# Kernel optimization log

Measured on AMD Instinct MI355X. Metric: run time of the kernel, lower is better.

The kernel has to match this reference:

```python
import jax, jax.numpy as jnp
import numpy as np

MATRIX_DIM = 128
FEAT = MATRIX_DIM * (MATRIX_DIM + 1) // 2  # 8256, triu incl. diagonal
HID = FEAT // 5                            # 1651
BATCH = 4096


def setup_inputs() -> dict:
    key = jax.random.key(0)
    k0, k1, k2, k3, k4 = jax.random.split(key, 5)
    stdv1 = 1.0 / FEAT / 2.0
    stdv2 = 1.0 / HID / 2.0
    return {
        "sim_matrices": jax.random.normal(k0, (BATCH, MATRIX_DIM, MATRIX_DIM), dtype=jnp.float32),
        "W1": jax.random.uniform(k1, (HID, FEAT), minval=-stdv1, maxval=stdv1, dtype=jnp.float32),
        "b1": jax.random.uniform(k2, (HID,), minval=-stdv1, maxval=stdv1, dtype=jnp.float32),
        "W2": jax.random.uniform(k3, (1, HID), minval=-stdv2, maxval=stdv2, dtype=jnp.float32),
        "b2": jax.random.uniform(k4, (1,), minval=-stdv2, maxval=stdv2, dtype=jnp.float32),
    }


def reference(sim_matrices, W1, b1, W2, b2):
    # flatten: take upper-triangular (incl. diag) entries -> [B, FEAT]
    iu0, iu1 = np.triu_indices(sim_matrices.shape[1])
    x = sim_matrices[:, iu0, iu1]
    # Linear_block 1 (ideal crossbar VMM = W x + b) + ReLU
    h = jax.nn.relu(jnp.einsum("bf,hf->bh", x, W1) + b1)
    # Linear_block 2 + Sigmoid -> [B, 1]
    return jax.nn.sigmoid(jnp.einsum("bh,oh->bo", h, W2) + b2)
```

## Files before the change

### kernel.cpp

```cpp
#include <hip/hip_runtime.h>
#include <hip/hip_bf16.h>
#include <math.h>

#define MDIM  128
#define FEAT  8256
#define HID   1651
#define HIDP  1664
#define BATCH 4096
#define BK    64
#define KT_TOTAL 129
#define NCHUNK 516
#define W1SCALE 8192.0f
#define W1INV   (1.0f / 8192.0f)
#define DEPTH 3

#define XT_CSTRIDE  ((i64)BATCH * 16)
#define W1T_CSTRIDE ((i64)HIDP * 16)

using f32x4  = __attribute__((ext_vector_type(4))) float;
using f32x16 = __attribute__((ext_vector_type(16))) float;
using i32x4  = __attribute__((ext_vector_type(4))) int;
using i32x8  = __attribute__((ext_vector_type(8))) int;
typedef long long i64;

__device__ __forceinline__ void gload_lds16(const void* g, void* l) {
    __builtin_amdgcn_global_load_lds(
        (const __attribute__((address_space(1))) void*)g,
        (__attribute__((address_space(3))) void*)l,
        16, 0, 0);
}

__device__ __forceinline__ int row_off(int i) { return (i * (257 - i)) >> 1; }

__device__ __forceinline__ void pack8_fp8(const float* f, int* o) {
    int lo = __builtin_amdgcn_cvt_pk_fp8_f32(f[0], f[1], 0, false);
    lo     = __builtin_amdgcn_cvt_pk_fp8_f32(f[2], f[3], lo, true);
    int hi = __builtin_amdgcn_cvt_pk_fp8_f32(f[4], f[5], 0, false);
    hi     = __builtin_amdgcn_cvt_pk_fp8_f32(f[6], f[7], hi, true);
    o[0] = lo; o[1] = hi;
}

__global__ void __launch_bounds__(256)
prep_kernel(const float* __restrict__ sim, const float* __restrict__ W1,
            char* __restrict__ Xt, char* __restrict__ W1t,
            float* __restrict__ out_pre) {
    const int t = threadIdx.x;
    if (blockIdx.x < BATCH) {
        const int b = blockIdx.x;
        const float* srow = sim + ((i64)b << 14);
#pragma unroll
        for (int it = 0; it < 5; ++it) {
            const int g = it * 256 + t;
            if (g < FEAT / 8) {
                const int f0 = g * 8;
                int i = (int)((257.0f - sqrtf(66049.0f - 8.0f * (float)f0)) * 0.5f);
                i = i < 0 ? 0 : (i > 127 ? 127 : i);
                while (i < 127 && row_off(i + 1) <= f0) ++i;
                while (i > 0 && row_off(i) > f0) --i;
                int j = i + (f0 - row_off(i));
                float v[8];
#pragma unroll
                for (int e = 0; e < 8; ++e) {
                    if (j > 127) { ++i; j = i; }
                    v[e] = srow[i * MDIM + j];
                    ++j;
                }
                int o[2];
                pack8_fp8(v, o);
                *(int2*)(Xt + (i64)(g >> 1) * XT_CSTRIDE + (i64)b * 16
                            + (g & 1) * 8) = make_int2(o[0], o[1]);
            }
        }
    } else if (blockIdx.x < BATCH + 5 * HIDP) {
        const int c  = blockIdx.x - BATCH;
        const int wb = c % 5;
        const int n  = c / 5;
        const int g  = wb * 256 + t;
        if (g >= FEAT / 8) return;
        const int f0 = g * 8;
        int o[2];
        if (n < HID) {
            const float* src = W1 + (i64)n * FEAT + f0;
            const f32x4 a = *(const f32x4*)src;
            const f32x4 d = *(const f32x4*)(src + 4);
            float v[8];
#pragma unroll
            for (int e = 0; e < 4; ++e) {
                v[e]     = a[e] * W1SCALE;
                v[e + 4] = d[e] * W1SCALE;
            }
            pack8_fp8(v, o);
        } else {
            o[0] = 0; o[1] = 0;
        }
        *(int2*)(W1t + (i64)(g >> 1) * W1T_CSTRIDE + (i64)n * 16
                    + (g & 1) * 8) = make_int2(o[0], o[1]);
    } else {
        const f32x4 zz = {0.f, 0.f, 0.f, 0.f};
        f32x4* p = (f32x4*)out_pre + t * 4;
        p[0] = zz; p[1] = zz; p[2] = zz; p[3] = zz;
    }
}

__global__ void __launch_bounds__(256, 3)
gemm_fused_kernel(const char* __restrict__ Xt,
                  const char* __restrict__ W1t,
                  const float* __restrict__ b1,
                  const float* __restrict__ W2,
                  float* __restrict__ out_pre) {
    __shared__ __align__(16) char lds_a[DEPTH * 8192];
    __shared__ __align__(16) char lds_b[DEPTH * 8192];

    const int t    = threadIdx.x;
    const int w    = t >> 6;
    const int l    = t & 63;
    const int bm   = blockIdx.x;
    const int bn   = blockIdx.y;
    const int wm   = w >> 1;
    const int wn   = w & 1;
    const int lm   = l & 31;
    const int c0   = (l >> 5) << 1;

    f32x16 acc[2][2];
#pragma unroll
    for (int r = 0; r < 16; ++r) {
        acc[0][0][r] = 0.f; acc[0][1][r] = 0.f;
        acc[1][0][r] = 0.f; acc[1][1][r] = 0.f;
    }

    const int nkt = KT_TOTAL;

    const char* gA0 = Xt + (i64)(w >> 1) * XT_CSTRIDE
                         + ((i64)bm * 128 + (w & 1) * 64 + l) * 16;
    const char* gB0 = W1t + (i64)(w >> 1) * W1T_CSTRIDE
                          + ((i64)bn * 128 + (w & 1) * 64 + l) * 16;
    char* lA = lds_a + w * 1024;
    char* lB = lds_b + w * 1024;

#define STAGE(buf, kidx) do {                                             \
        const char* _ga = gA0 + (i64)(kidx) * (4 * XT_CSTRIDE);           \
        const char* _gb = gB0 + (i64)(kidx) * (4 * W1T_CSTRIDE);          \
        char* _la = lA + (buf) * 8192;                                    \
        char* _lb = lB + (buf) * 8192;                                    \
        gload_lds16(_ga,                    _la);                         \
        gload_lds16(_ga + 2 * XT_CSTRIDE,   _la + 4096);                  \
        gload_lds16(_gb,                    _lb);                         \
        gload_lds16(_gb + 2 * W1T_CSTRIDE,  _lb + 4096);                  \
    } while (0)

    STAGE(0, 0);
    STAGE(1, 1);
    STAGE(2, 2);

    int cur = 0;
    for (int kt = 0; kt < nkt; ++kt) {
        if (kt + 3 <= nkt)      asm volatile("s_waitcnt vmcnt(8)" ::: "memory");
        else if (kt + 2 == nkt) asm volatile("s_waitcnt vmcnt(4)" ::: "memory");
        else                    asm volatile("s_waitcnt vmcnt(0)" ::: "memory");
        __builtin_amdgcn_s_barrier();
        __builtin_amdgcn_sched_barrier(0);

        const char* pa = lds_a + cur * 8192 + c0 * 2048 + (wm * 64 + lm) * 16;
        const char* pb = lds_b + cur * 8192 + c0 * 2048 + (wn * 64 + lm) * 16;
        i32x8 A0, A1, B0, B1;
        *((i32x4*)&A0)     = *(const i32x4*)(pa);
        *((i32x4*)&A0 + 1) = *(const i32x4*)(pa + 2048);
        *((i32x4*)&A1)     = *(const i32x4*)(pa + 512);
        *((i32x4*)&A1 + 1) = *(const i32x4*)(pa + 512 + 2048);
        *((i32x4*)&B0)     = *(const i32x4*)(pb);
        *((i32x4*)&B0 + 1) = *(const i32x4*)(pb + 2048);
        *((i32x4*)&B1)     = *(const i32x4*)(pb + 512);
        *((i32x4*)&B1 + 1) = *(const i32x4*)(pb + 512 + 2048);

        __builtin_amdgcn_s_setprio(1);
        acc[0][0] = __builtin_amdgcn_mfma_scale_f32_32x32x64_f8f6f4(
            A0, B0, acc[0][0], 0, 0, 0, 0x7F7F7F7F, 0, 0x7F7F7F7F);
        acc[0][1] = __builtin_amdgcn_mfma_scale_f32_32x32x64_f8f6f4(
            A0, B1, acc[0][1], 0, 0, 0, 0x7F7F7F7F, 0, 0x7F7F7F7F);
        acc[1][0] = __builtin_amdgcn_mfma_scale_f32_32x32x64_f8f6f4(
            A1, B0, acc[1][0], 0, 0, 0, 0x7F7F7F7F, 0, 0x7F7F7F7F);
        acc[1][1] = __builtin_amdgcn_mfma_scale_f32_32x32x64_f8f6f4(
            A1, B1, acc[1][1], 0, 0, 0, 0x7F7F7F7F, 0, 0x7F7F7F7F);
        __builtin_amdgcn_s_setprio(0);

        asm volatile("s_waitcnt lgkmcnt(0)" ::: "memory");
        __builtin_amdgcn_sched_barrier(0);
        __builtin_amdgcn_s_barrier();
        __builtin_amdgcn_sched_barrier(0);

        if (kt + 3 < nkt) STAGE(cur, kt + 3);
        cur = (cur == DEPTH - 1) ? 0 : cur + 1;
    }
#undef STAGE

    const int colbase = bn * 128 + wn * 64 + lm;
    float b1v[2], w2v[2];
#pragma unroll
    for (int cb = 0; cb < 2; ++cb) {
        const int col = colbase + cb * 32;
        const bool ok = col < HID;
        b1v[cb] = ok ? b1[col] : 0.f;
        w2v[cb] = ok ? W2[col] : 0.f;
    }
    const int rbase = bm * 128 + wm * 64 + ((l >> 5) << 2);
#pragma unroll
    for (int rb = 0; rb < 2; ++rb)
#pragma unroll
        for (int reg = 0; reg < 16; ++reg) {
            float v = 0.f;
#pragma unroll
            for (int cb = 0; cb < 2; ++cb) {
                const float pre = acc[rb][cb][reg] * W1INV + b1v[cb];
                v += fmaxf(pre, 0.f) * w2v[cb];
            }
            v += __shfl_xor(v, 1);
            v += __shfl_xor(v, 2);
            v += __shfl_xor(v, 4);
            v += __shfl_xor(v, 8);
            v += __shfl_xor(v, 16);
            if (lm == 0) {
                const int row = rbase + rb * 32 + (reg & 3) + ((reg >> 2) << 3);
                atomicAdd(out_pre + row, v);
            }
        }
}

__global__ void __launch_bounds__(256)
sigmoid_kernel(const float* __restrict__ pre,
               const float* __restrict__ b2,
               float* __restrict__ out) {
    const int i = blockIdx.x * 256 + threadIdx.x;
    out[i] = 1.0f / (1.0f + expf(-(pre[i] + b2[0])));
}

extern "C" void kernel_launch(void* const* d_in, const int* in_sizes, int n_in,
                              void* d_out, int out_size, void* d_ws, size_t ws_size,
                              hipStream_t stream) {
    const float* sim = (const float*)d_in[0];
    const float* W1  = (const float*)d_in[1];
    const float* b1  = (const float*)d_in[2];
    const float* W2  = (const float*)d_in[3];
    const float* b2  = (const float*)d_in[4];
    float* out = (float*)d_out;

    char* ws = (char*)d_ws;
    const i64 X_OFF   = 0;
    const i64 W1P_OFF = (i64)BATCH * FEAT;
    const i64 PRE_OFF = W1P_OFF + (i64)HIDP * FEAT;
    char*  Xt   = ws + X_OFF;
    char*  W1t  = ws + W1P_OFF;
    float* pre  = (float*)(ws + PRE_OFF);

    prep_kernel<<<BATCH + 5 * HIDP + 1, 256, 0, stream>>>(sim, W1, Xt, W1t, pre);
    {
        dim3 grid(BATCH / 128, HIDP / 128);
        gemm_fused_kernel<<<grid, 256, 0, stream>>>(Xt, W1t, b1, W2, pre);
    }
    sigmoid_kernel<<<BATCH / 256, 256, 0, stream>>>(pre, b2, out);
}
```

Before: 482.8 us.

## Load A operand directly to registers in MFMA-fragment layout, bypassing LDS

The prep kernel now writes the fp8 activation matrix in a layout where each wave's MFMA A fragment is contiguous per k-step. The GEMM kernel loads A straight from global memory into registers, triple-buffered two k-steps ahead, while only B still goes through LDS. This halves LDS traffic and footprint and drops the A LDS round trip. In exchange it depends on global load latency being hidden by register prefetch, and it adds VGPR pressure from six extra 8-wide register buffers.

```diff
diff --git a/kernel.cpp b/kernel.cpp
--- a/kernel.cpp
+++ b/kernel.cpp
@@ -9,13 +9,11 @@
 #define BATCH 4096
 #define BK    64
 #define KT_TOTAL 129
-#define NCHUNK 516
 #define W1SCALE 8192.0f
 #define W1INV   (1.0f / 8192.0f)
-#define DEPTH 3
-
-#define XT_CSTRIDE  ((i64)BATCH * 16)
+
 #define W1T_CSTRIDE ((i64)HIDP * 16)
+#define XA_KSTEP ((i64)128 * 2048)
 
 using f32x4  = __attribute__((ext_vector_type(4))) float;
 using f32x16 = __attribute__((ext_vector_type(16))) float;
@@ -42,12 +40,14 @@
 
 __global__ void __launch_bounds__(256)
 prep_kernel(const float* __restrict__ sim, const float* __restrict__ W1,
-            char* __restrict__ Xt, char* __restrict__ W1t,
+            char* __restrict__ XA, char* __restrict__ W1t,
             float* __restrict__ out_pre) {
     const int t = threadIdx.x;
     if (blockIdx.x < BATCH) {
         const int b = blockIdx.x;
         const float* srow = sim + ((i64)b << 14);
+        const int mg   = b >> 5;
+        const int brow = b & 31;
 #pragma unroll
         for (int it = 0; it < 5; ++it) {
             const int g = it * 256 + t;
@@ -67,8 +67,13 @@
                 }
                 int o[2];
                 pack8_fp8(v, o);
-                *(int2*)(Xt + (i64)(g >> 1) * XT_CSTRIDE + (i64)b * 16
-                            + (g & 1) * 8) = make_int2(o[0], o[1]);
+                const int kt   = f0 >> 6;
+                const int k64  = f0 & 63;
+                const int lane = brow | ((k64 >> 5) << 5);
+                const int h    = (k64 >> 4) & 1;
+                const i64 off  = ((i64)(kt * 128 + mg) * 2 + h) * 1024
+                               + lane * 16 + (k64 & 15);
+                *(int2*)(XA + off) = make_int2(o[0], o[1]);
             }
         }
     } else if (blockIdx.x < BATCH + 5 * HIDP) {
@@ -103,13 +108,12 @@
 }
 
 __global__ void __launch_bounds__(256, 3)
-gemm_fused_kernel(const char* __restrict__ Xt,
+gemm_fused_kernel(const char* __restrict__ XA,
                   const char* __restrict__ W1t,
                   const float* __restrict__ b1,
                   const float* __restrict__ W2,
                   float* __restrict__ out_pre) {
-    __shared__ __align__(16) char lds_a[DEPTH * 8192];
-    __shared__ __align__(16) char lds_b[DEPTH * 8192];
+    __shared__ __align__(16) char lds_b[3 * 8192];
 
     const int t    = threadIdx.x;
     const int w    = t >> 6;
@@ -128,70 +132,81 @@
         acc[1][0][r] = 0.f; acc[1][1][r] = 0.f;
     }
 
-    const int nkt = KT_TOTAL;
-
-    const char* gA0 = Xt + (i64)(w >> 1) * XT_CSTRIDE
-                         + ((i64)bm * 128 + (w & 1) * 64 + l) * 16;
+    const char* pA0 = XA + (i64)(bm * 4 + wm * 2) * 2048 + l * 16;
+
     const char* gB0 = W1t + (i64)(w >> 1) * W1T_CSTRIDE
                           + ((i64)bn * 128 + (w & 1) * 64 + l) * 16;
-    char* lA = lds_a + w * 1024;
     char* lB = lds_b + w * 1024;
 
-#define STAGE(buf, kidx) do {                                             \
-        const char* _ga = gA0 + (i64)(kidx) * (4 * XT_CSTRIDE);           \
+#define STAGE_B(slot, kidx) do {                                          \
         const char* _gb = gB0 + (i64)(kidx) * (4 * W1T_CSTRIDE);          \
-        char* _la = lA + (buf) * 8192;                                    \
-        char* _lb = lB + (buf) * 8192;                                    \
-        gload_lds16(_ga,                    _la);                         \
-        gload_lds16(_ga + 2 * XT_CSTRIDE,   _la + 4096);                  \
-        gload_lds16(_gb,                    _lb);                         \
-        gload_lds16(_gb + 2 * W1T_CSTRIDE,  _lb + 4096);                  \
-    } while (0)
-
-    STAGE(0, 0);
-    STAGE(1, 1);
-    STAGE(2, 2);
-
-    int cur = 0;
-    for (int kt = 0; kt < nkt; ++kt) {
-        if (kt + 3 <= nkt)      asm volatile("s_waitcnt vmcnt(8)" ::: "memory");
-        else if (kt + 2 == nkt) asm volatile("s_waitcnt vmcnt(4)" ::: "memory");
-        else                    asm volatile("s_waitcnt vmcnt(0)" ::: "memory");
-        __builtin_amdgcn_s_barrier();
-        __builtin_amdgcn_sched_barrier(0);
-
-        const char* pa = lds_a + cur * 8192 + c0 * 2048 + (wm * 64 + lm) * 16;
-        const char* pb = lds_b + cur * 8192 + c0 * 2048 + (wn * 64 + lm) * 16;
-        i32x8 A0, A1, B0, B1;
-        *((i32x4*)&A0)     = *(const i32x4*)(pa);
-        *((i32x4*)&A0 + 1) = *(const i32x4*)(pa + 2048);
-        *((i32x4*)&A1)     = *(const i32x4*)(pa + 512);
-        *((i32x4*)&A1 + 1) = *(const i32x4*)(pa + 512 + 2048);
-        *((i32x4*)&B0)     = *(const i32x4*)(pb);
-        *((i32x4*)&B0 + 1) = *(const i32x4*)(pb + 2048);
-        *((i32x4*)&B1)     = *(const i32x4*)(pb + 512);
-        *((i32x4*)&B1 + 1) = *(const i32x4*)(pb + 512 + 2048);
-
-        __builtin_amdgcn_s_setprio(1);
-        acc[0][0] = __builtin_amdgcn_mfma_scale_f32_32x32x64_f8f6f4(
-            A0, B0, acc[0][0], 0, 0, 0, 0x7F7F7F7F, 0, 0x7F7F7F7F);
-        acc[0][1] = __builtin_amdgcn_mfma_scale_f32_32x32x64_f8f6f4(
-            A0, B1, acc[0][1], 0, 0, 0, 0x7F7F7F7F, 0, 0x7F7F7F7F);
-        acc[1][0] = __builtin_amdgcn_mfma_scale_f32_32x32x64_f8f6f4(
-            A1, B0, acc[1][0], 0, 0, 0, 0x7F7F7F7F, 0, 0x7F7F7F7F);
-        acc[1][1] = __builtin_amdgcn_mfma_scale_f32_32x32x64_f8f6f4(
-            A1, B1, acc[1][1], 0, 0, 0, 0x7F7F7F7F, 0, 0x7F7F7F7F);
-        __builtin_amdgcn_s_setprio(0);
-
-        asm volatile("s_waitcnt lgkmcnt(0)" ::: "memory");
-        __builtin_amdgcn_sched_barrier(0);
-        __builtin_amdgcn_s_barrier();
-        __builtin_amdgcn_sched_barrier(0);
-
-        if (kt + 3 < nkt) STAGE(cur, kt + 3);
-        cur = (cur == DEPTH - 1) ? 0 : cur + 1;
-    }
-#undef STAGE
+        char* _lb = lB + (slot) * 8192;                                   \
+        gload_lds16(_gb,                   _lb);                          \
+        gload_lds16(_gb + 2 * W1T_CSTRIDE, _lb + 4096);                   \
+    } while (0)
+
+#define LOAD_A(kt, an0, an1) do {                                         \
+        const char* _pa = pA0 + (i64)(kt) * XA_KSTEP;                     \
+        *((i32x4*)&(an0))     = *(const i32x4*)(_pa);                     \
+        *((i32x4*)&(an0) + 1) = *(const i32x4*)(_pa + 1024);              \
+        *((i32x4*)&(an1))     = *(const i32x4*)(_pa + 2048);              \
+        *((i32x4*)&(an1) + 1) = *(const i32x4*)(_pa + 3072);              \
+    } while (0)
+
+#define MFMA4(a0, a1, B0, B1) do {                                        \
+        __builtin_amdgcn_s_setprio(1);                                    \
+        acc[0][0] = __builtin_amdgcn_mfma_scale_f32_32x32x64_f8f6f4(      \
+            (a0), (B0), acc[0][0], 0, 0, 0, 0x7F7F7F7F, 0, 0x7F7F7F7F);   \
+        acc[0][1] = __builtin_amdgcn_mfma_scale_f32_32x32x64_f8f6f4(      \
+            (a0), (B1), acc[0][1], 0, 0, 0, 0x7F7F7F7F, 0, 0x7F7F7F7F);   \
+        acc[1][0] = __builtin_amdgcn_mfma_scale_f32_32x32x64_f8f6f4(      \
+            (a1), (B0), acc[1][0], 0, 0, 0, 0x7F7F7F7F, 0, 0x7F7F7F7F);   \
+        acc[1][1] = __builtin_amdgcn_mfma_scale_f32_32x32x64_f8f6f4(      \
+            (a1), (B1), acc[1][1], 0, 0, 0, 0x7F7F7F7F, 0, 0x7F7F7F7F);   \
+        __builtin_amdgcn_s_setprio(0);                                    \
+    } while (0)
+
+#define ITER(kt, slot, ac0, ac1, an0, an1, DOLOAD, DOSTAGE, WAIT) do {    \
+        asm volatile("s_waitcnt vmcnt(" WAIT ")" ::: "memory");           \
+        __builtin_amdgcn_s_barrier();           \
+        __builtin_amdgcn_sched_barrier(0);                                \
+        const char* _pb = lds_b + (slot) * 8192 + c0 * 2048               \
+                        + (wn * 64 + lm) * 16;                            \
+        i32x8 B0, B1;                                                     \
+        *((i32x4*)&B0)     = *(const i32x4*)(_pb);                        \
+        *((i32x4*)&B0 + 1) = *(const i32x4*)(_pb + 2048);                 \
+        *((i32x4*)&B1)     = *(const i32x4*)(_pb + 512);                  \
+        *((i32x4*)&B1 + 1) = *(const i32x4*)(_pb + 512 + 2048);           \
+        if (DOLOAD) LOAD_A((kt) + 2, an0, an1);                           \
+        MFMA4(ac0, ac1, B0, B1);                                          \
+        asm volatile("s_waitcnt lgkmcnt(0)" ::: "memory");                \
+        __builtin_amdgcn_sched_barrier(0);                                \
+        __builtin_amdgcn_s_barrier();            \
+        __builtin_amdgcn_sched_barrier(0);                                \
+        if (DOSTAGE) STAGE_B(slot, (kt) + 3);                             \
+    } while (0)
+
+    i32x8 a0A, a1A, a0B, a1B, a0C, a1C;
+
+    STAGE_B(0, 0);
+    STAGE_B(1, 1);
+    LOAD_A(0, a0A, a1A);
+    LOAD_A(1, a0B, a1B);
+    STAGE_B(2, 2);
+
+    for (int kt3 = 0; kt3 < 126; kt3 += 3) {
+        ITER(kt3 + 0, 0, a0A, a1A, a0C, a1C, 1, 1, "6");
+        ITER(kt3 + 1, 1, a0B, a1B, a0A, a1A, 1, 1, "6");
+        ITER(kt3 + 2, 2, a0C, a1C, a0B, a1B, 1, 1, "6");
+    }
+    ITER(126, 0, a0A, a1A, a0C, a1C, 1, 0, "6");
+    ITER(127, 1, a0B, a1B, a0A, a1A, 0, 0, "4");
+    ITER(128, 2, a0C, a1C, a0A, a1A, 0, 0, "0");
+
+#undef ITER
+#undef MFMA4
+#undef LOAD_A
+#undef STAGE_B
 
     const int colbase = bn * 128 + wn * 64 + lm;
     float b1v[2], w2v[2];
@@ -247,14 +262,14 @@
     const i64 X_OFF   = 0;
     const i64 W1P_OFF = (i64)BATCH * FEAT;
     const i64 PRE_OFF = W1P_OFF + (i64)HIDP * FEAT;
-    char*  Xt   = ws + X_OFF;
+    char*  XA   = ws + X_OFF;
     char*  W1t  = ws + W1P_OFF;
     float* pre  = (float*)(ws + PRE_OFF);
 
-    prep_kernel<<<BATCH + 5 * HIDP + 1, 256, 0, stream>>>(sim, W1, Xt, W1t, pre);
+    prep_kernel<<<BATCH + 5 * HIDP + 1, 256, 0, stream>>>(sim, W1, XA, W1t, pre);
     {
         dim3 grid(BATCH / 128, HIDP / 128);
-        gemm_fused_kernel<<<grid, 256, 0, stream>>>(Xt, W1t, b1, W2, pre);
+        gemm_fused_kernel<<<grid, 256, 0, stream>>>(XA, W1t, b1, W2, pre);
     }
     sigmoid_kernel<<<BATCH / 256, 256, 0, stream>>>(pre, b2, out);
 }
```

Result: no change. 478.0 us (-1.0%).
